# Kernel optimization log

Measured on AMD Instinct MI355X. Metric: run time of the kernel, lower is better.

The kernel has to match this reference:

```python
import jax, jax.numpy as jnp
import numpy as np

GAMMA = 0.99
RHO_THRESHOLD = 1.0
C_THRESHOLD = 1.0
BASELINE_LOSS_SCALING = 0.5
ENT_COEFF = 0.01
PPO_CLIP = 0.2


def setup_inputs() -> dict:
    key = jax.random.key(0)
    ks = jax.random.split(key, 7)
    T, B, A = 512, 8192, 2
    return {
        "prob": jax.random.uniform(ks[0], (T, B, A), dtype=jnp.float32),
        "action_prob": jax.random.uniform(ks[1], (T, B, A), dtype=jnp.float32),
        "v": jax.random.normal(ks[2], (T, B), dtype=jnp.float32),
        "next_v": jax.random.normal(ks[3], (T, B), dtype=jnp.float32),
        "reward": jax.random.normal(ks[4], (T, B), dtype=jnp.float32),
        "action": jax.random.randint(ks[5], (T, B), 0, 2, dtype=jnp.int32),
        "done": jax.random.randint(ks[6], (T, B), 0, 2, dtype=jnp.int32),
    }


def _log_prob(p, a):
    # torch.distributions.Categorical normalizes unnormalized probs
    logp = jnp.log(p) - jnp.log(p.sum(-1, keepdims=True))  # [T,B,A]
    return jnp.take_along_axis(logp, a[..., None].astype(jnp.int32), axis=-1)[..., 0]


def reference(prob, action_prob, v, next_v, reward, action, done):
    done_f = done.astype(v.dtype)  # [T,B]
    logp = _log_prob(prob, action)
    logp_act = _log_prob(action_prob, action)
    ratio = jnp.exp(logp - logp_act)  # [T,B]

    clipped_rho = jnp.minimum(ratio, RHO_THRESHOLD)
    clipped_c = jnp.minimum(ratio, C_THRESHOLD)
    deltas = clipped_rho * (reward + (1.0 - done_f) * GAMMA * next_v - v)

    # V-trace backward recurrence over time (dim 0), vectorized over batch
    def step(next_vtrace, xs):
        v_t, d_t, c_t, rho_t, r_t, nv_t, dn_t = xs
        vt = v_t + d_t + GAMMA * c_t * (next_vtrace - nv_t) * (1.0 - dn_t)
        adv = rho_t * (r_t + GAMMA * next_vtrace * (1.0 - dn_t) - v_t)
        return vt, (vt, adv)

    _, (vtrace, adv) = jax.lax.scan(
        step, next_v[-1],
        (v, deltas, clipped_c, clipped_rho, reward, next_v, done_f),
        reverse=True)

    vtrace = jax.lax.stop_gradient(vtrace)  # .detach() in original
    adv = jax.lax.stop_gradient(adv)

    critic_loss = BASELINE_LOSS_SCALING * jnp.mean((v - vtrace) ** 2)
    surr1 = ratio * adv
    surr2 = jnp.clip(ratio, 1.0 - PPO_CLIP, 1.0 + PPO_CLIP) * adv
    actor_loss = -jnp.minimum(surr1, surr2).mean()

    # entropy is logged but NOT included in total_loss in the original
    total_loss = actor_loss + critic_loss
    return total_loss
```

## Files before the change

kernel.cpp:

```cpp
#include <hip/hip_runtime.h>

#define T_DIM 512
#define B_DIM 8192
#define NCH   16
#define LT    32
#define CG    64
#define NCG   (B_DIM / CG)
#define WPB   8
#define K_BLOCK (WPB * 64)
#define K_GRID  ((NCH * NCG) / WPB)
#define GAMMA 0.99f

#define SM_OFF  0
#define CIN_OFF (NCH * B_DIM * sizeof(float2))
#define ACC_OFF (CIN_OFF + NCH * B_DIM * sizeof(float))


__device__ __forceinline__ void eval_t(const float2 pr, const float2 qr,
                                       const float vv, const float rr,
                                       const int a, const int d,
                                       float& ratio, float& m, float& s) {
    float pa = a ? pr.y : pr.x;
    float qa = a ? qr.y : qr.x;
    ratio = (pa * (qr.x + qr.y)) / ((pr.x + pr.y) * qa);
    float rho = fminf(ratio, 1.0f);
    m = d ? 0.0f : GAMMA * rho;
    s = fmaf(rho, rr - vv, vv);
}

__launch_bounds__(K_BLOCK, 4)
__global__ void k_comp(const float* __restrict__ prob,
                       const float* __restrict__ aprob,
                       const float* __restrict__ v,
                       const float* __restrict__ rw,
                       const int* __restrict__ act,
                       const int* __restrict__ dnn,
                       float2* __restrict__ SM) {
    const int lane = threadIdx.x & 63;
    const int gw   = blockIdx.x * WPB + (threadIdx.x >> 6);
    const int cg   = gw & (NCG - 1);
    const int ch   = gw >> 7;
    const int col  = cg * CG + lane;
    const int t0   = ch * LT;

    const float2* __restrict__ prob2  = (const float2*)prob;
    const float2* __restrict__ aprob2 = (const float2*)aprob;

    float S = 0.0f, M = 1.0f;
#pragma unroll 4
    for (int i = LT - 1; i >= 0; --i) {
        const int idx = (t0 + i) * B_DIM + col;
        float ratio, m, s;
        eval_t(prob2[idx], aprob2[idx], v[idx], rw[idx], act[idx], dnn[idx],
               ratio, m, s);
        S = fmaf(m, S, s);
        M *= m;
    }
    SM[ch * B_DIM + col] = make_float2(S, M);
}

__global__ void k_scan(const float2* __restrict__ SM,
                       const float* __restrict__ nv,
                       float* __restrict__ CIN) {
    const int col = blockIdx.x * blockDim.x + threadIdx.x;
    float carry = nv[(T_DIM - 1) * B_DIM + col];
#pragma unroll
    for (int ch = NCH - 1; ch >= 0; --ch) {
        float2 sm = SM[ch * B_DIM + col];
        CIN[ch * B_DIM + col] = carry;
        carry = fmaf(sm.y, carry, sm.x);
    }
}

__launch_bounds__(K_BLOCK, 4)
__global__ void k_replay(const float* __restrict__ prob,
                         const float* __restrict__ aprob,
                         const float* __restrict__ v,
                         const float* __restrict__ rw,
                         const int* __restrict__ act,
                         const int* __restrict__ dnn,
                         const float* __restrict__ CIN,
                         float* __restrict__ ACC,
                         float* __restrict__ out) {
    __shared__ float red[2 * WPB];
    const int lane = threadIdx.x & 63;
    const int wv   = threadIdx.x >> 6;
    const int gw   = blockIdx.x * WPB + wv;
    const int cg   = gw & (NCG - 1);
    const int ch   = gw >> 7;
    const int col  = cg * CG + lane;
    const int t0   = ch * LT;

    const float2* __restrict__ prob2  = (const float2*)prob;
    const float2* __restrict__ aprob2 = (const float2*)aprob;

    float carry  = CIN[ch * B_DIM + col];
    float critic = 0.0f, msum = 0.0f;
#pragma unroll 4
    for (int i = LT - 1; i >= 0; --i) {
        const int idx = (t0 + i) * B_DIM + col;
        float ratio, m, s;
        eval_t(prob2[idx], aprob2[idx], v[idx], rw[idx], act[idx], dnn[idx],
               ratio, m, s);
        float u   = fmaf(m, carry, s);
        float adv = u - v[idx];
        carry     = u;
        critic = fmaf(adv, adv, critic);
        float rc = fminf(fmaxf(ratio, 0.8f), 1.2f);
        msum += fminf(ratio * adv, rc * adv);
    }

#pragma unroll
    for (int off = 32; off > 0; off >>= 1) {
        critic += __shfl_down(critic, off, 64);
        msum   += __shfl_down(msum, off, 64);
    }
    if (lane == 0) { red[wv] = critic; red[WPB + wv] = msum; }
    __syncthreads();
    if (threadIdx.x == 0) {
        float cs = 0.0f, ms = 0.0f;
#pragma unroll
        for (int w = 0; w < WPB; ++w) { cs += red[w]; ms += red[WPB + w]; }
        atomicAdd(&ACC[0], cs);
        atomicAdd(&ACC[1], ms);
        __threadfence();
        unsigned* cnt = (unsigned*)(ACC + 2);
        if (atomicAdd(cnt, 1u) == K_GRID - 1) {
            __threadfence();
            float c_tot = atomicAdd(&ACC[0], 0.0f);
            float m_tot = atomicAdd(&ACC[1], 0.0f);
            const float invN = 1.0f / (float)((size_t)T_DIM * B_DIM);
            out[0] = 0.5f * c_tot * invN - m_tot * invN;
        }
    }
}

extern "C" void kernel_launch(void* const* d_in, const int* in_sizes, int n_in,
                              void* d_out, int out_size, void* d_ws, size_t ws_size,
                              hipStream_t stream) {
    const float* prob  = (const float*)d_in[0];
    const float* aprob = (const float*)d_in[1];
    const float* v     = (const float*)d_in[2];
    const float* nv    = (const float*)d_in[3];
    const float* rw    = (const float*)d_in[4];
    const int*   act   = (const int*)d_in[5];
    const int*   dnn   = (const int*)d_in[6];

    float2* SM  = (float2*)((char*)d_ws + SM_OFF);
    float*  CIN = (float*)((char*)d_ws + CIN_OFF);
    float*  ACC = (float*)((char*)d_ws + ACC_OFF);
    float*  out = (float*)d_out;

    hipMemsetAsync(ACC, 0, 12, stream);
    k_comp<<<K_GRID, K_BLOCK, 0, stream>>>(prob, aprob, v, rw, act, dnn, SM);
    k_scan<<<B_DIM / 256, 256, 0, stream>>>(SM, nv, CIN);
    k_replay<<<K_GRID, K_BLOCK, 0, stream>>>(prob, aprob, v, rw, act, dnn,
                                             CIN, ACC, out);
}
```

Measured before the change: 189.4 us.

## Vectorize chunked V-trace kernels to four columns per lane with shorter chunks

Each lane now handles four adjacent batch columns with float4/int4 loads instead of one column with scalar or float2 loads. The time chunk length drops from 32 to 4, giving 128 chunks, and the block shape changes to match. The per-chunk S and M summaries go into separate arrays, and the scan writes carry-ins over S in place. The aim is wider memory transactions and more parallel work in the two streaming passes. The cost is a serial scan over 128 chunks per column, with more intermediate traffic and a longer dependent chain in k_scan.

```diff
diff --git a/kernel.cpp b/kernel.cpp
--- a/kernel.cpp
+++ b/kernel.cpp
@@ -2,27 +2,26 @@
 
 #define T_DIM 512
 #define B_DIM 8192
-#define NCH   16
-#define LT    32
-#define CG    64
-#define NCG   (B_DIM / CG)
-#define WPB   8
-#define K_BLOCK (WPB * 64)
+#define NCH   128
+#define LT    4
+#define CPW   256
+#define NCG   (B_DIM / CPW)
+#define WPB   4
+#define K_BLOCK 256
 #define K_GRID  ((NCH * NCG) / WPB)
 #define GAMMA 0.99f
 
-#define SM_OFF  0
-#define CIN_OFF (NCH * B_DIM * sizeof(float2))
-#define ACC_OFF (CIN_OFF + NCH * B_DIM * sizeof(float))
-
-
-__device__ __forceinline__ void eval_t(const float2 pr, const float2 qr,
-                                       const float vv, const float rr,
-                                       const int a, const int d,
-                                       float& ratio, float& m, float& s) {
-    float pa = a ? pr.y : pr.x;
-    float qa = a ? qr.y : qr.x;
-    ratio = (pa * (qr.x + qr.y)) / ((pr.x + pr.y) * qa);
+#define SC_OFF  0
+#define MM_OFF  ((size_t)NCH * B_DIM * sizeof(float))
+#define ACC_OFF (2 * MM_OFF)
+
+
+__device__ __forceinline__ void col_eval(float p0, float p1, float q0, float q1,
+                                         float vv, float rr, int a, int d,
+                                         float& ratio, float& m, float& s) {
+    float pa = a ? p1 : p0;
+    float qa = a ? q1 : q0;
+    ratio = (pa * (q0 + q1)) / ((p0 + p1) * qa);
     float rho = fminf(ratio, 1.0f);
     m = d ? 0.0f : GAMMA * rho;
     s = fmaf(rho, rr - vv, vv);
@@ -35,40 +34,62 @@
                        const float* __restrict__ rw,
                        const int* __restrict__ act,
                        const int* __restrict__ dnn,
-                       float2* __restrict__ SM) {
+                       float* __restrict__ SC,
+                       float* __restrict__ MM) {
     const int lane = threadIdx.x & 63;
     const int gw   = blockIdx.x * WPB + (threadIdx.x >> 6);
     const int cg   = gw & (NCG - 1);
-    const int ch   = gw >> 7;
-    const int col  = cg * CG + lane;
+    const int ch   = gw >> 5;
+    const int col4 = cg * 64 + lane;
     const int t0   = ch * LT;
 
-    const float2* __restrict__ prob2  = (const float2*)prob;
-    const float2* __restrict__ aprob2 = (const float2*)aprob;
-
-    float S = 0.0f, M = 1.0f;
-#pragma unroll 4
+    const float4* __restrict__ prob4  = (const float4*)prob;
+    const float4* __restrict__ aprob4 = (const float4*)aprob;
+    const float4* __restrict__ v4     = (const float4*)v;
+    const float4* __restrict__ rw4    = (const float4*)rw;
+    const int4*   __restrict__ act4   = (const int4*)act;
+    const int4*   __restrict__ dnn4   = (const int4*)dnn;
+
+    float S0 = 0.f, S1 = 0.f, S2 = 0.f, S3 = 0.f;
+    float M0 = 1.f, M1 = 1.f, M2 = 1.f, M3 = 1.f;
+#pragma unroll
     for (int i = LT - 1; i >= 0; --i) {
-        const int idx = (t0 + i) * B_DIM + col;
+        const int t  = t0 + i;
+        const int rb = t * (B_DIM / 4) + col4;
+        const int pb = t * (B_DIM / 2) + col4 * 2;
+        float4 pr0 = prob4[pb],  pr1 = prob4[pb + 1];
+        float4 qr0 = aprob4[pb], qr1 = aprob4[pb + 1];
+        float4 vv  = v4[rb];
+        float4 rr  = rw4[rb];
+        int4   aa  = act4[rb];
+        int4   dd  = dnn4[rb];
         float ratio, m, s;
-        eval_t(prob2[idx], aprob2[idx], v[idx], rw[idx], act[idx], dnn[idx],
-               ratio, m, s);
-        S = fmaf(m, S, s);
-        M *= m;
-    }
-    SM[ch * B_DIM + col] = make_float2(S, M);
-}
-
-__global__ void k_scan(const float2* __restrict__ SM,
-                       const float* __restrict__ nv,
-                       float* __restrict__ CIN) {
+        col_eval(pr0.x, pr0.y, qr0.x, qr0.y, vv.x, rr.x, aa.x, dd.x, ratio, m, s);
+        S0 = fmaf(m, S0, s); M0 *= m;
+        col_eval(pr0.z, pr0.w, qr0.z, qr0.w, vv.y, rr.y, aa.y, dd.y, ratio, m, s);
+        S1 = fmaf(m, S1, s); M1 *= m;
+        col_eval(pr1.x, pr1.y, qr1.x, qr1.y, vv.z, rr.z, aa.z, dd.z, ratio, m, s);
+        S2 = fmaf(m, S2, s); M2 *= m;
+        col_eval(pr1.z, pr1.w, qr1.z, qr1.w, vv.w, rr.w, aa.w, dd.w, ratio, m, s);
+        S3 = fmaf(m, S3, s); M3 *= m;
+    }
+    float4* SC4 = (float4*)SC;
+    float4* MM4 = (float4*)MM;
+    SC4[ch * (B_DIM / 4) + col4] = make_float4(S0, S1, S2, S3);
+    MM4[ch * (B_DIM / 4) + col4] = make_float4(M0, M1, M2, M3);
+}
+
+__global__ void k_scan(float* __restrict__ SC,
+                       const float* __restrict__ MM,
+                       const float* __restrict__ nv) {
     const int col = blockIdx.x * blockDim.x + threadIdx.x;
     float carry = nv[(T_DIM - 1) * B_DIM + col];
-#pragma unroll
+#pragma unroll 16
     for (int ch = NCH - 1; ch >= 0; --ch) {
-        float2 sm = SM[ch * B_DIM + col];
-        CIN[ch * B_DIM + col] = carry;
-        carry = fmaf(sm.y, carry, sm.x);
+        float s = SC[ch * B_DIM + col];
+        float m = MM[ch * B_DIM + col];
+        SC[ch * B_DIM + col] = carry;
+        carry = fmaf(m, carry, s);
     }
 }
 
@@ -87,26 +108,56 @@
     const int wv   = threadIdx.x >> 6;
     const int gw   = blockIdx.x * WPB + wv;
     const int cg   = gw & (NCG - 1);
-    const int ch   = gw >> 7;
-    const int col  = cg * CG + lane;
+    const int ch   = gw >> 5;
+    const int col4 = cg * 64 + lane;
     const int t0   = ch * LT;
 
-    const float2* __restrict__ prob2  = (const float2*)prob;
-    const float2* __restrict__ aprob2 = (const float2*)aprob;
-
-    float carry  = CIN[ch * B_DIM + col];
+    const float4* __restrict__ prob4  = (const float4*)prob;
+    const float4* __restrict__ aprob4 = (const float4*)aprob;
+    const float4* __restrict__ v4     = (const float4*)v;
+    const float4* __restrict__ rw4    = (const float4*)rw;
+    const int4*   __restrict__ act4   = (const int4*)act;
+    const int4*   __restrict__ dnn4   = (const int4*)dnn;
+    const float4* __restrict__ cin4   = (const float4*)CIN;
+
+    float4 cc = cin4[ch * (B_DIM / 4) + col4];
+    float c0 = cc.x, c1 = cc.y, c2 = cc.z, c3 = cc.w;
     float critic = 0.0f, msum = 0.0f;
-#pragma unroll 4
+#pragma unroll
     for (int i = LT - 1; i >= 0; --i) {
-        const int idx = (t0 + i) * B_DIM + col;
-        float ratio, m, s;
-        eval_t(prob2[idx], aprob2[idx], v[idx], rw[idx], act[idx], dnn[idx],
-               ratio, m, s);
-        float u   = fmaf(m, carry, s);
-        float adv = u - v[idx];
-        carry     = u;
-        critic = fmaf(adv, adv, critic);
-        float rc = fminf(fmaxf(ratio, 0.8f), 1.2f);
+        const int t  = t0 + i;
+        const int rb = t * (B_DIM / 4) + col4;
+        const int pb = t * (B_DIM / 2) + col4 * 2;
+        float4 pr0 = prob4[pb],  pr1 = prob4[pb + 1];
+        float4 qr0 = aprob4[pb], qr1 = aprob4[pb + 1];
+        float4 vv  = v4[rb];
+        float4 rr  = rw4[rb];
+        int4   aa  = act4[rb];
+        int4   dd  = dnn4[rb];
+        float ratio, m, s, u, adv, rc;
+
+        col_eval(pr0.x, pr0.y, qr0.x, qr0.y, vv.x, rr.x, aa.x, dd.x, ratio, m, s);
+        u = fmaf(m, c0, s); adv = u - vv.x; c0 = u;
+        critic = fmaf(adv, adv, critic);
+        rc = fminf(fmaxf(ratio, 0.8f), 1.2f);
+        msum += fminf(ratio * adv, rc * adv);
+
+        col_eval(pr0.z, pr0.w, qr0.z, qr0.w, vv.y, rr.y, aa.y, dd.y, ratio, m, s);
+        u = fmaf(m, c1, s); adv = u - vv.y; c1 = u;
+        critic = fmaf(adv, adv, critic);
+        rc = fminf(fmaxf(ratio, 0.8f), 1.2f);
+        msum += fminf(ratio * adv, rc * adv);
+
+        col_eval(pr1.x, pr1.y, qr1.x, qr1.y, vv.z, rr.z, aa.z, dd.z, ratio, m, s);
+        u = fmaf(m, c2, s); adv = u - vv.z; c2 = u;
+        critic = fmaf(adv, adv, critic);
+        rc = fminf(fmaxf(ratio, 0.8f), 1.2f);
+        msum += fminf(ratio * adv, rc * adv);
+
+        col_eval(pr1.z, pr1.w, qr1.z, qr1.w, vv.w, rr.w, aa.w, dd.w, ratio, m, s);
+        u = fmaf(m, c3, s); adv = u - vv.w; c3 = u;
+        critic = fmaf(adv, adv, critic);
+        rc = fminf(fmaxf(ratio, 0.8f), 1.2f);
         msum += fminf(ratio * adv, rc * adv);
     }
 
@@ -118,9 +169,8 @@
     if (lane == 0) { red[wv] = critic; red[WPB + wv] = msum; }
     __syncthreads();
     if (threadIdx.x == 0) {
-        float cs = 0.0f, ms = 0.0f;
-#pragma unroll
-        for (int w = 0; w < WPB; ++w) { cs += red[w]; ms += red[WPB + w]; }
+        float cs = red[0] + red[1] + red[2] + red[3];
+        float ms = red[WPB] + red[WPB + 1] + red[WPB + 2] + red[WPB + 3];
         atomicAdd(&ACC[0], cs);
         atomicAdd(&ACC[1], ms);
         __threadfence();
@@ -146,14 +196,14 @@
     const int*   act   = (const int*)d_in[5];
     const int*   dnn   = (const int*)d_in[6];
 
-    float2* SM  = (float2*)((char*)d_ws + SM_OFF);
-    float*  CIN = (float*)((char*)d_ws + CIN_OFF);
-    float*  ACC = (float*)((char*)d_ws + ACC_OFF);
-    float*  out = (float*)d_out;
+    float* SC  = (float*)((char*)d_ws + SC_OFF);
+    float* MM  = (float*)((char*)d_ws + MM_OFF);
+    float* ACC = (float*)((char*)d_ws + ACC_OFF);
+    float* out = (float*)d_out;
 
     hipMemsetAsync(ACC, 0, 12, stream);
-    k_comp<<<K_GRID, K_BLOCK, 0, stream>>>(prob, aprob, v, rw, act, dnn, SM);
-    k_scan<<<B_DIM / 256, 256, 0, stream>>>(SM, nv, CIN);
+    k_comp<<<K_GRID, K_BLOCK, 0, stream>>>(prob, aprob, v, rw, act, dnn, SC, MM);
+    k_scan<<<B_DIM / 256, 256, 0, stream>>>(SC, MM, nv);
     k_replay<<<K_GRID, K_BLOCK, 0, stream>>>(prob, aprob, v, rw, act, dnn,
-                                             CIN, ACC, out);
-}
+                                             SC, ACC, out);
+}
```

Result: slower. 223.5 us (+18.0%).
